# Kernel optimization log

Measured on AMD Instinct MI355X. Metric: run time of the kernel, lower is better.

## Reference

```python
import jax, jax.numpy as jnp
import numpy as np

DIM = 1024
HEADS = 16
HEAD_DIM = DIM // HEADS
B, S = 2, 2048


def setup_inputs() -> dict:
    key = jax.random.key(0)
    ks = jax.random.split(key, 12)
    scale = 1.0 / np.sqrt(DIM)
    inp = {
        "Q_in": jax.random.normal(ks[0], (B, S, DIM), jnp.float32),
        "K_in": jax.random.normal(ks[1], (B, S, DIM), jnp.float32),
        "V_in": jax.random.normal(ks[2], (B, S, DIM), jnp.float32),
        "Wq": jax.random.normal(ks[3], (DIM, DIM), jnp.float32) * scale,
        "bq": jnp.zeros((DIM,), jnp.float32),
        "Wk": jax.random.normal(ks[4], (DIM, DIM), jnp.float32) * scale,
        "bk": jnp.zeros((DIM,), jnp.float32),
        "Wv": jax.random.normal(ks[5], (DIM, DIM), jnp.float32) * scale,
        "bv": jnp.zeros((DIM,), jnp.float32),
        "Wo": jax.random.normal(ks[6], (DIM, DIM), jnp.float32) * scale,
        "bo": jnp.zeros((DIM,), jnp.float32),
        "is_causal": 1,
    }
    return inp


def reference(Q_in, K_in, V_in, Wq, bq, Wk, bk, Wv, bv, Wo, bo, is_causal):
    b, s, d = Q_in.shape
    hd = d // HEADS
    # linear projections (torch nn.Linear: x @ W.T + b), split heads -> [b,h,s,hd]
    Q = (Q_in @ Wq.T + bq).reshape(b, s, HEADS, hd).transpose(0, 2, 1, 3)
    K = (K_in @ Wk.T + bk).reshape(b, s, HEADS, hd).transpose(0, 2, 1, 3)
    V = (V_in @ Wv.T + bv).reshape(b, s, HEADS, hd).transpose(0, 2, 1, 3)
    # full [b,h,s,s] score matrix, as in the original (no fused SDPA)
    scores = jnp.einsum("bhqd,bhkd->bhqk", Q, K) / jnp.sqrt(jnp.float32(hd))
    if is_causal:
        causal = jnp.tril(jnp.ones((s, s), dtype=bool))  # [s,s]
        scores = jnp.where(causal, scores, jnp.float32(-jnp.inf))
    attn = jax.nn.softmax(scores, axis=-1)
    # dropout is identity (eval mode) for a deterministic reference
    out = jnp.einsum("bhqk,bhkd->bhqd", attn, V)
    out = out.transpose(0, 2, 1, 3).reshape(b, s, d)
    return out @ Wo.T + bo
```

## Files before the change

kernel.cpp:

```cpp
#include <hip/hip_runtime.h>
#include <hip/hip_bf16.h>
#include <stdint.h>

#define HEADS 16
#define HD 64
#define BATCH 2
#define SEQ 2048
#define NDIM 1024
#define MROWS (BATCH * SEQ)

typedef __attribute__((ext_vector_type(8))) __bf16 bf16x8;
typedef __attribute__((ext_vector_type(4))) __bf16 bf16x4;
typedef __attribute__((ext_vector_type(4))) float f32x4;

#define LOG2E 1.4426950408889634f
#define SOFTMAX_C 16.0f

#if __has_builtin(__builtin_amdgcn_exp2f)
#define EXP2(x) __builtin_amdgcn_exp2f(x)
#else
#define EXP2(x) exp2f(x)
#endif

#define GLDS16(g, l)                                                          \
  __builtin_amdgcn_global_load_lds(                                           \
      (const __attribute__((address_space(1))) unsigned int*)(g),             \
      (__attribute__((address_space(3))) unsigned int*)(l), 16, 0, 0)

__global__ void cvt_all_kernel(const float* __restrict__ xq, const float* __restrict__ xk,
                               const float* __restrict__ xv, const float* __restrict__ wq,
                               const float* __restrict__ wk, const float* __restrict__ wv,
                               const float* __restrict__ wo,
                               __bf16* __restrict__ oxq, __bf16* __restrict__ oxk,
                               __bf16* __restrict__ oxv, __bf16* __restrict__ owq,
                               __bf16* __restrict__ owk, __bf16* __restrict__ owv,
                               __bf16* __restrict__ owo) {
  const int id = blockIdx.x;
  const float* in;
  __bf16* out;
  int blk;
  if (id < 12288) {
    const int m = id >> 12;
    blk = id & 4095;
    in = (m == 0) ? xq : (m == 1) ? xk : xv;
    out = (m == 0) ? oxq : (m == 1) ? oxk : oxv;
  } else {
    const int m = (id - 12288) >> 10;
    blk = (id - 12288) & 1023;
    in = (m == 0) ? wq : (m == 1) ? wk : (m == 2) ? wv : wo;
    out = (m == 0) ? owq : (m == 1) ? owk : (m == 2) ? owv : owo;
  }
  const size_t i = ((size_t)blk * 256 + threadIdx.x) * 4;
  const float4 v = *(const float4*)(in + i);
  bf16x4 o = {(__bf16)v.x, (__bf16)v.y, (__bf16)v.z, (__bf16)v.w};
  *(bf16x4*)(out + i) = o;
}

template <int BNF, bool TRC>
__device__ __forceinline__ void gemm_core(const __bf16* __restrict__ A,
                                          const __bf16* __restrict__ B,
                                          int m0, int n0,
                                          char* lA, char* lB,
                                          f32x4 acc[4][BNF]) {
  constexpr int BBUF = BNF * 2048;
  constexpr int NLD = (BNF == 4) ? 4 : 3;
  const int t = threadIdx.x;
  const int lane = t & 63;
  const int llo = lane & 15, lhi = lane >> 4;
  const int wid = t >> 6;
  const int wrow = (wid >> 1) * 64;
  const int wcol = (wid & 1) * (BNF * 16);

  const int rA = t >> 2;
  const int cA = (t & 3) * 8;

  const __bf16* pA0 = A + (size_t)(m0 + rA) * 1024 + cA;
  const __bf16* pA1 = A + (size_t)(m0 + 64 + rA) * 1024 + cA;
  const __bf16* pB0 = B + (size_t)(n0 + rA) * 1024 + cA;
  const __bf16* pB1 = B + (size_t)(n0 + (BNF == 4 ? 64 : 0) + rA) * 1024 + cA;

#pragma unroll
  for (int mf = 0; mf < 4; ++mf)
#pragma unroll
    for (int nf = 0; nf < BNF; ++nf)
      acc[mf][nf] = (f32x4){0.f, 0.f, 0.f, 0.f};

#define STAGE_G(buf, k0)                                                      \
  do {                                                                        \
    GLDS16(pA0 + (k0), lA + (buf) * 8192 + t * 16);                           \
    GLDS16(pA1 + (k0), lA + (buf) * 8192 + 4096 + t * 16);                    \
    GLDS16(pB0 + (k0), lB + (buf) * BBUF + t * 16);                           \
    if (BNF == 4) GLDS16(pB1 + (k0), lB + (buf) * BBUF + 4096 + t * 16);      \
  } while (0)

  STAGE_G(0, 0);
  STAGE_G(1, 32);

  int cb = 0;
  for (int k0 = 0; k0 < 1024; k0 += 32) {
    const int step = k0 >> 5;
    if (step + 2 < 32) {
      const int sb = (cb >= 1) ? (cb - 1) : (cb + 2);
      STAGE_G(sb, k0 + 64);
      asm volatile("s_waitcnt vmcnt(%0)" :: "i"(2 * NLD) : "memory");
    } else if (step + 1 < 32) {
      asm volatile("s_waitcnt vmcnt(%0)" :: "i"(NLD) : "memory");
    } else {
      asm volatile("s_waitcnt vmcnt(0)" ::: "memory");
    }
    __builtin_amdgcn_s_barrier();
    __builtin_amdgcn_sched_barrier(0);

    bf16x8 af[4], bfr[BNF];
#pragma unroll
    for (int mf = 0; mf < 4; ++mf)
      af[mf] = *(const bf16x8*)(lA + cb * 8192 +
                                ((wrow + mf * 16 + llo) * 32 + lhi * 8) * 2);
#pragma unroll
    for (int nf = 0; nf < BNF; ++nf)
      bfr[nf] = *(const bf16x8*)(lB + cb * BBUF +
                                 ((wcol + nf * 16 + llo) * 32 + lhi * 8) * 2);
    __builtin_amdgcn_s_setprio(1);
#pragma unroll
    for (int mf = 0; mf < 4; ++mf)
#pragma unroll
      for (int nf = 0; nf < BNF; ++nf)
        acc[mf][nf] = TRC
            ? __builtin_amdgcn_mfma_f32_16x16x32_bf16(bfr[nf], af[mf],
                                                      acc[mf][nf], 0, 0, 0)
            : __builtin_amdgcn_mfma_f32_16x16x32_bf16(af[mf], bfr[nf],
                                                      acc[mf][nf], 0, 0, 0);
    __builtin_amdgcn_s_setprio(0);
    __builtin_amdgcn_s_barrier();
    cb = (cb == 2) ? 0 : (cb + 1);
  }
#undef STAGE_G
}

__global__ __launch_bounds__(256, 3)
void qkv_gemm_kernel(const __bf16* __restrict__ Xq, const __bf16* __restrict__ Xk,
                     const __bf16* __restrict__ Xv, const __bf16* __restrict__ Wq,
                     const __bf16* __restrict__ Wk, const __bf16* __restrict__ Wv,
                     const float* __restrict__ bq, const float* __restrict__ bk,
                     const float* __restrict__ bv, __bf16* __restrict__ Qh,
                     __bf16* __restrict__ Kh, __bf16* __restrict__ Vt) {
  __shared__ __align__(16) char ldsA[3 * 8192];
  __shared__ __align__(16) char ldsB[3 * 8192];

  const int lid = blockIdx.x;
  const int xcd = lid & 7, slot = lid >> 3;
  const int y = xcd + 8 * (slot >> 5);
  const int x = slot & 31;
  const int m0 = x * 128;
  const int mat = y >> 3;
  const int n0 = (y & 7) * 128;

  const __bf16* A = (mat == 0) ? Xq : (mat == 1) ? Xk : Xv;
  const __bf16* B = (mat == 0) ? Wq : (mat == 1) ? Wk : Wv;
  const float* bias = (mat == 0) ? bq : (mat == 1) ? bk : bv;

  const int t = threadIdx.x;
  const int lane = t & 63;
  const int llo = lane & 15, lhi = lane >> 4;
  const int wid = t >> 6;
  const int wrow = (wid >> 1) * 64;
  const int wcol = (wid & 1) * 64;

  f32x4 acc[4][4];
  if (mat < 2) {
    gemm_core<4, true>(A, B, m0, n0, ldsA, ldsB, acc);
    __bf16* dst = (mat == 0) ? Qh : Kh;
    const float qs = (mat == 0) ? (0.125f * LOG2E) : 1.0f;
#pragma unroll
    for (int nf = 0; nf < 4; ++nf) {
      const int cbase = n0 + wcol + nf * 16 + lhi * 4;
      const float4 b4 = *(const float4*)(bias + cbase);
      const int h = cbase >> 6, d0 = cbase & 63;
#pragma unroll
      for (int mf = 0; mf < 4; ++mf) {
        const int sg = m0 + wrow + mf * 16 + llo;
        const int b = sg >> 11, s0 = sg & 2047;
        bf16x4 pk;
        pk[0] = (__bf16)((acc[mf][nf][0] + b4.x) * qs);
        pk[1] = (__bf16)((acc[mf][nf][1] + b4.y) * qs);
        pk[2] = (__bf16)((acc[mf][nf][2] + b4.z) * qs);
        pk[3] = (__bf16)((acc[mf][nf][3] + b4.w) * qs);
        *(bf16x4*)(dst + ((size_t)(b * HEADS + h) * SEQ + s0) * HD + d0) = pk;
      }
    }
  } else {
    gemm_core<4, false>(A, B, m0, n0, ldsA, ldsB, acc);
#pragma unroll
    for (int nf = 0; nf < 4; ++nf) {
      const int cfull = n0 + wcol + nf * 16 + llo;
      const int h = cfull >> 6, d = cfull & 63;
      const float bb = bias[cfull];
#pragma unroll
      for (int mf = 0; mf < 4; ++mf) {
        const int row0 = m0 + wrow + mf * 16 + lhi * 4;
        const int b = row0 >> 11;
        const int s0 = row0 & 2047;
        bf16x4 pk;
#pragma unroll
        for (int j = 0; j < 4; ++j) pk[j] = (__bf16)(acc[mf][nf][j] + bb);
        *(bf16x4*)(Vt + ((size_t)(b * HEADS + h) * HD + d) * SEQ + s0) = pk;
      }
    }
  }
}

__global__ __launch_bounds__(256, 4)
void attn_kernel(const __bf16* __restrict__ Qh, const __bf16* __restrict__ Kh,
                 const __bf16* __restrict__ Vt, __bf16* __restrict__ O,
                 const int* __restrict__ causal_flag) {
  __shared__ __align__(16) __bf16 kbuf[2][64 * 64];
  __shared__ __align__(16) __bf16 vbuf[2][64 * 64];
  __shared__ __align__(16) __bf16 pbuf[4][16 * 64];

  const int t = threadIdx.x;
  const int lane = t & 63;
  const int llo = lane & 15, lhi = lane >> 4;
  const int w = t >> 6;
  const int causal = causal_flag[0];

  const int lid = blockIdx.x;
  const int xcd = lid & 7, slot = lid >> 3;
  const int group = slot >> 5, r = slot & 31;
  const int bh = xcd + 8 * group;
  const int b = bh >> 4, h = bh & 15;
  const int rr = (group >= 2) ? ((r + 8) & 31) : r;
  const int qt = (group & 1) ? (31 - rr) : rr;

  const __bf16* Qb = Qh + (size_t)bh * SEQ * HD;
  const __bf16* Kb = Kh + (size_t)bh * SEQ * HD;
  const __bf16* Vb = Vt + (size_t)bh * HD * SEQ;

  const int sr = t >> 3;
  const int sce = (((t & 7) * 16) ^ ((sr & 7) << 4)) >> 1;
  const int swz = (llo & 7) << 4;

  char* const pw = (char*)&pbuf[w][0];

  const int qw = qt * 64 + w * 16;
  const int nt = causal ? (qt + 1) : (SEQ / 64);

  bf16x8 bQ[2];
#pragma unroll
  for (int ks = 0; ks < 2; ++ks)
    bQ[ks] = *(const bf16x8*)(Qb + (size_t)(qw + llo) * HD + ks * 32 + lhi * 8);

  float lrun = 0.f;
  f32x4 accO[4];
#pragma unroll
  for (int nf = 0; nf < 4; ++nf) accO[nf] = (f32x4){0.f, 0.f, 0.f, 0.f};

  GLDS16(Kb + (size_t)sr * HD + sce,        (char*)&kbuf[0][0] + t * 16);
  GLDS16(Kb + (size_t)(32 + sr) * HD + sce, (char*)&kbuf[0][0] + 4096 + t * 16);
  GLDS16(Vb + (size_t)sr * SEQ + sce,       (char*)&vbuf[0][0] + t * 16);
  GLDS16(Vb + (size_t)(32 + sr) * SEQ + sce,(char*)&vbuf[0][0] + 4096 + t * 16);
  __syncthreads();
  int cur = 0;

  for (int tkv = 0; tkv < nt; ++tkv) {
    if (tkv + 1 < nt) {
      const int k0s = (tkv + 1) * 64;
      char* kd = (char*)&kbuf[cur ^ 1][0];
      char* vd = (char*)&vbuf[cur ^ 1][0];
      GLDS16(Kb + (size_t)(k0s + sr) * HD + sce,        kd + t * 16);
      GLDS16(Kb + (size_t)(k0s + 32 + sr) * HD + sce,   kd + 4096 + t * 16);
      GLDS16(Vb + (size_t)sr * SEQ + k0s + sce,         vd + t * 16);
      GLDS16(Vb + (size_t)(32 + sr) * SEQ + k0s + sce,  vd + 4096 + t * 16);
    }
    const int k0 = tkv * 64;
    const char* kb = (const char*)&kbuf[cur][0];
    const char* vb = (const char*)&vbuf[cur][0];

    f32x4 s[4];
#pragma unroll
    for (int nf = 0; nf < 4; ++nf) s[nf] = (f32x4){0.f, 0.f, 0.f, 0.f};
    __builtin_amdgcn_s_setprio(1);
#pragma unroll
    for (int ks = 0; ks < 2; ++ks)
#pragma unroll
      for (int nf = 0; nf < 4; ++nf) {
        bf16x8 aK = *(const bf16x8*)(kb + (nf * 16 + llo) * 128 +
                                     ((ks * 64 + lhi * 16) ^ swz));
        s[nf] = __builtin_amdgcn_mfma_f32_16x16x32_bf16(aK, bQ[ks], s[nf], 0, 0, 0);
      }
    __builtin_amdgcn_s_setprio(0);

    if (causal && tkv == qt) {
      const int qrow = qw + llo;
#pragma unroll
      for (int nf = 0; nf < 4; ++nf)
#pragma unroll
        for (int j = 0; j < 4; ++j)
          if (k0 + nf * 16 + lhi * 4 + j > qrow) s[nf][j] = -1e30f;
    }

#pragma unroll
    for (int nf = 0; nf < 4; ++nf)
#pragma unroll
      for (int j = 0; j < 4; ++j) {
        const float pv = EXP2(s[nf][j] - SOFTMAX_C);
        s[nf][j] = pv;
        lrun += pv;
      }

#pragma unroll
    for (int nf = 0; nf < 4; ++nf) {
      bf16x4 pk = {(__bf16)s[nf][0], (__bf16)s[nf][1], (__bf16)s[nf][2],
                   (__bf16)s[nf][3]};
      *(bf16x4*)(pw + llo * 128 + ((32 * nf + 8 * lhi) ^ swz)) = pk;
    }
    __builtin_amdgcn_s_setprio(1);
#pragma unroll
    for (int ks2 = 0; ks2 < 2; ++ks2) {
      bf16x8 bP = *(const bf16x8*)(pw + llo * 128 + ((64 * ks2 + 16 * lhi) ^ swz));
#pragma unroll
      for (int nf = 0; nf < 4; ++nf) {
        bf16x8 aV = *(const bf16x8*)(vb + (nf * 16 + llo) * 128 +
                                     ((64 * ks2 + 16 * lhi) ^ swz));
        accO[nf] = __builtin_amdgcn_mfma_f32_16x16x32_bf16(aV, bP, accO[nf], 0, 0, 0);
      }
    }
    __builtin_amdgcn_s_setprio(0);
    __syncthreads();
    cur ^= 1;
  }

  lrun += __shfl_xor(lrun, 16, 64);
  lrun += __shfl_xor(lrun, 32, 64);
  const float linv = 1.f / lrun;
  const int srow = qw + llo;
#pragma unroll
  for (int nf = 0; nf < 4; ++nf) {
    bf16x4 pk;
#pragma unroll
    for (int j = 0; j < 4; ++j) pk[j] = (__bf16)(accO[nf][j] * linv);
    *(bf16x4*)(O + ((size_t)(b * SEQ + srow) * HEADS + h) * HD + nf * 16 +
               lhi * 4) = pk;
  }
}

__global__ __launch_bounds__(256, 4)
void out_gemm_kernel(const __bf16* __restrict__ Oin, const __bf16* __restrict__ Wo,
                     const float* __restrict__ bo, float* __restrict__ out) {
  __shared__ __align__(16) char ldsA[3 * 8192];
  __shared__ __align__(16) char ldsB[3 * 4096];

  const int lid = blockIdx.x;
  const int xcd = lid & 7, slot = lid >> 3;
  const int n0 = (xcd + 8 * (slot >> 5)) * 64;
  const int m0 = (slot & 31) * 128;

  f32x4 acc[4][2];
  gemm_core<2, false>(Oin, Wo, m0, n0, ldsA, ldsB, acc);

  const int t = threadIdx.x;
  const int lane = t & 63;
  const int llo = lane & 15, lhi = lane >> 4;
  const int wid = t >> 6;
  const int wrow = (wid >> 1) * 64;
  const int wcol = (wid & 1) * 32;

#pragma unroll
  for (int nf = 0; nf < 2; ++nf) {
    const int col = n0 + wcol + nf * 16 + llo;
    const float bb = bo[col];
#pragma unroll
    for (int mf = 0; mf < 4; ++mf)
#pragma unroll
      for (int j = 0; j < 4; ++j) {
        const int row = m0 + wrow + mf * 16 + lhi * 4 + j;
        out[(size_t)row * NDIM + col] = acc[mf][nf][j] + bb;
      }
  }
}

extern "C" void kernel_launch(void* const* d_in, const int* in_sizes, int n_in,
                              void* d_out, int out_size, void* d_ws, size_t ws_size,
                              hipStream_t stream) {
  const float* Q_in = (const float*)d_in[0];
  const float* K_in = (const float*)d_in[1];
  const float* V_in = (const float*)d_in[2];
  const float* Wq = (const float*)d_in[3];
  const float* bq = (const float*)d_in[4];
  const float* Wk = (const float*)d_in[5];
  const float* bk = (const float*)d_in[6];
  const float* Wv = (const float*)d_in[7];
  const float* bv = (const float*)d_in[8];
  const float* Wo = (const float*)d_in[9];
  const float* bo = (const float*)d_in[10];
  const int* causal = (const int*)d_in[11];
  float* out = (float*)d_out;

  char* p = (char*)d_ws;
  const size_t SZ_X = (size_t)MROWS * NDIM * 2;
  const size_t SZ_W = (size_t)NDIM * NDIM * 2;
  __bf16* bXq = (__bf16*)p; p += SZ_X;
  __bf16* bXk = (__bf16*)p; p += SZ_X;
  __bf16* bXv = (__bf16*)p; p += SZ_X;
  __bf16* bWq = (__bf16*)p; p += SZ_W;
  __bf16* bWk = (__bf16*)p; p += SZ_W;
  __bf16* bWv = (__bf16*)p; p += SZ_W;
  __bf16* bWo = (__bf16*)p; p += SZ_W;
  __bf16* Qh  = (__bf16*)p; p += SZ_X;
  __bf16* Kh  = (__bf16*)p; p += SZ_X;
  __bf16* Vt  = (__bf16*)p; p += SZ_X;
  __bf16* Obf = (__bf16*)p; p += SZ_X;

  cvt_all_kernel<<<16384, 256, 0, stream>>>(Q_in, K_in, V_in, Wq, Wk, Wv, Wo,
                                            bXq, bXk, bXv, bWq, bWk, bWv, bWo);

  qkv_gemm_kernel<<<768, 256, 0, stream>>>(bXq, bXk, bXv, bWq, bWk, bWv,
                                           bq, bk, bv, Qh, Kh, Vt);
  attn_kernel<<<1024, 256, 0, stream>>>(Qh, Kh, Vt, Obf, causal);
  out_gemm_kernel<<<512, 256, 0, stream>>>(Obf, bWo, bo, out);
}
```

Measured before the change: 118.0 us.

## Swizzle GEMM LDS tile layout and remap blocks to XCDs by M rows

The global-to-LDS staging now writes each 32-column bf16 tile with an XOR swizzle: two rows share a 128-byte line and the 16-byte chunk index is permuted. The fragment reads use the matching swizzled address, with the aim of removing LDS bank conflicts on the MFMA operand loads. Block-to-tile mapping in the QKV and output GEMMs is also changed so each XCD owns a contiguous band of M rows across all N tiles, which should improve L2 reuse of the A operand. The risk is that a wrong swizzle silently corrupts results, and the new mapping shifts reuse from the weight matrix to the activations.

```diff
diff --git a/kernel.cpp b/kernel.cpp
--- a/kernel.cpp
+++ b/kernel.cpp
@@ -71,13 +71,14 @@
   const int wrow = (wid >> 1) * 64;
   const int wcol = (wid & 1) * (BNF * 16);
 
-  const int rA = t >> 2;
-  const int cA = (t & 3) * 8;
-
-  const __bf16* pA0 = A + (size_t)(m0 + rA) * 1024 + cA;
-  const __bf16* pA1 = A + (size_t)(m0 + 64 + rA) * 1024 + cA;
-  const __bf16* pB0 = B + (size_t)(n0 + rA) * 1024 + cA;
-  const __bf16* pB1 = B + (size_t)(n0 + (BNF == 4 ? 64 : 0) + rA) * 1024 + cA;
+  const int sl = (t & 7) ^ ((t >> 3) & 7);
+  const int srg = 2 * (t >> 3) + (sl >> 2);
+  const int cg = (sl & 3) * 8;
+
+  const __bf16* pA0 = A + (size_t)(m0 + srg) * 1024 + cg;
+  const __bf16* pA1 = A + (size_t)(m0 + 64 + srg) * 1024 + cg;
+  const __bf16* pB0 = B + (size_t)(n0 + srg) * 1024 + cg;
+  const __bf16* pB1 = B + (size_t)(n0 + (BNF == 4 ? 64 : 0) + srg) * 1024 + cg;
 
 #pragma unroll
   for (int mf = 0; mf < 4; ++mf)
@@ -95,6 +96,8 @@
 
   STAGE_G(0, 0);
   STAGE_G(1, 32);
+
+  const int fcol = ((((llo & 1) << 2) | lhi) ^ (llo >> 1)) << 4;
 
   int cb = 0;
   for (int k0 = 0; k0 < 1024; k0 += 32) {
@@ -113,13 +116,15 @@
 
     bf16x8 af[4], bfr[BNF];
 #pragma unroll
-    for (int mf = 0; mf < 4; ++mf)
-      af[mf] = *(const bf16x8*)(lA + cb * 8192 +
-                                ((wrow + mf * 16 + llo) * 32 + lhi * 8) * 2);
-#pragma unroll
-    for (int nf = 0; nf < BNF; ++nf)
-      bfr[nf] = *(const bf16x8*)(lB + cb * BBUF +
-                                 ((wcol + nf * 16 + llo) * 32 + lhi * 8) * 2);
+    for (int mf = 0; mf < 4; ++mf) {
+      const int R = wrow + mf * 16 + llo;
+      af[mf] = *(const bf16x8*)(lA + cb * 8192 + (R >> 1) * 128 + fcol);
+    }
+#pragma unroll
+    for (int nf = 0; nf < BNF; ++nf) {
+      const int R = wcol + nf * 16 + llo;
+      bfr[nf] = *(const bf16x8*)(lB + cb * BBUF + (R >> 1) * 128 + fcol);
+    }
     __builtin_amdgcn_s_setprio(1);
 #pragma unroll
     for (int mf = 0; mf < 4; ++mf)
@@ -149,9 +154,8 @@
 
   const int lid = blockIdx.x;
   const int xcd = lid & 7, slot = lid >> 3;
-  const int y = xcd + 8 * (slot >> 5);
-  const int x = slot & 31;
-  const int m0 = x * 128;
+  const int y = slot >> 2;
+  const int m0 = (xcd * 4 + (slot & 3)) * 128;
   const int mat = y >> 3;
   const int n0 = (y & 7) * 128;
 
@@ -351,8 +355,8 @@
 
   const int lid = blockIdx.x;
   const int xcd = lid & 7, slot = lid >> 3;
-  const int n0 = (xcd + 8 * (slot >> 5)) * 64;
-  const int m0 = (slot & 31) * 128;
+  const int n0 = (slot >> 2) * 64;
+  const int m0 = (xcd * 4 + (slot & 3)) * 128;
 
   f32x4 acc[4][2];
   gemm_core<2, false>(Oin, Wo, m0, n0, ldsA, ldsB, acc);
```

After: 112.4 us. 1.05x faster.
